# Performance work log

Hardware: AMD Instinct MI355X
Metric: run time of the kernel (lower is better)

The kernel has to match this reference:

```python
import jax, jax.numpy as jnp
import numpy as np

N_NODES = 100000


def gcn_conv(x, edge_index, W, b):
    # PyG GCNConv: add self-loops, symmetric normalization, then scatter-add.
    n = x.shape[0]
    loops = jnp.arange(n, dtype=edge_index.dtype)
    src = jnp.concatenate([edge_index[0], loops])
    dst = jnp.concatenate([edge_index[1], loops])
    h = x @ W  # [N, F_out] -- transform before propagate (small GEMM)
    ones = jnp.ones(src.shape[0], dtype=x.dtype)
    deg = jax.ops.segment_sum(ones, dst, num_segments=n)  # in-degree incl. self-loop
    dinv = jnp.where(deg > 0, jax.lax.rsqrt(deg), 0.0)
    norm = dinv[src] * dinv[dst]  # [E+N]
    msg = h[src] * norm[:, None]  # gather + scale, [E+N, F_out]
    out = jax.ops.segment_sum(msg, dst, num_segments=n)  # scatter-add
    return out + b


def setup_inputs() -> dict:
    key = jax.random.key(0)
    k1, k2, k3, k4 = jax.random.split(key, 4)
    d = 128
    x = jax.random.normal(k1, (N_NODES, d), dtype=jnp.float32)
    edge_index = jax.random.randint(k2, (2, 1600000), 0, N_NODES, dtype=jnp.int64)
    scale = 1.0 / np.sqrt(d)
    W1 = jax.random.normal(k3, (d, d), dtype=jnp.float32) * scale
    b1 = jnp.zeros((d,), dtype=jnp.float32)
    W2 = jax.random.normal(k4, (d, d), dtype=jnp.float32) * scale
    b2 = jnp.zeros((d,), dtype=jnp.float32)
    return {"x": x, "edge_index": edge_index, "W1": W1, "b1": b1, "W2": W2, "b2": b2}


def reference(x, edge_index, W1, b1, W2, b2):
    # Layer 1: GCNConv -> relu -> dropout(eval: identity)
    h = jax.nn.relu(gcn_conv(x, edge_index, W1, b1))
    # Layer 2
    h = jax.nn.relu(gcn_conv(h, edge_index, W2, b2))
    return h
```

## Files before the change

### kernel.cpp

```cpp
#include <hip/hip_runtime.h>


#define NFEAT 128
#define BSH 7
#define MAXNB 1024
#define BCAP 4096
#define BPITCH 136

typedef __attribute__((ext_vector_type(8))) short s8v;
typedef __attribute__((ext_vector_type(4))) float f4v;
typedef __attribute__((ext_vector_type(2))) float f2v;

__device__ inline ushort f2bf(float f) {
    union { float f; uint u; } x; x.f = f;
    uint u = x.u;
    return (ushort)((u + 0x7fffu + ((u >> 16) & 1u)) >> 16);
}
__device__ inline float bf16lo(uint u) { union { uint u; float f; } x; x.u = u << 16; return x.f; }
__device__ inline float bf16hi(uint u) { union { uint u; float f; } x; x.u = u & 0xffff0000u; return x.f; }
__device__ inline f2v unpk(uint u) {
    union { uint u; float f; } lo, hi;
    lo.u = u << 16;
    hi.u = u & 0xffff0000u;
    return (f2v){lo.f, hi.f};
}
__device__ inline void upadd2(uint4 v, f2v* a) {
    a[0] += unpk(v.x);
    a[1] += unpk(v.y);
    a[2] += unpk(v.z);
    a[3] += unpk(v.w);
}

__global__ __launch_bounds__(256) void k_bscatter(const int* __restrict__ src,
                                                  const int* __restrict__ dst,
                                                  int* __restrict__ gcnt,
                                                  uint* __restrict__ ebuf,
                                                  int E, int NB, int CH) {
    __shared__ int h[MAXNB];
    int t = threadIdx.x;
    for (int i = t; i < NB; i += 256) h[i] = 0;
    __syncthreads();
    int e0 = blockIdx.x * CH;
    int e1 = min(e0 + CH, E);
    for (int e = e0 + t; e < e1; e += 256) atomicAdd(&h[dst[e] >> BSH], 1);
    __syncthreads();
    for (int i = t; i < NB; i += 256) {
        int c = h[i];
        h[i] = c ? (i * BCAP + atomicAdd(&gcnt[i], c)) : 0;
    }
    __syncthreads();
    for (int e = e0 + t; e < e1; e += 256) {
        int d = dst[e];
        int b = d >> BSH;
        int p = atomicAdd(&h[b], 1);
        if (p < (b + 1) * BCAP)
            ebuf[p] = ((uint)src[e] << BSH) | (uint)(d & ((1 << BSH) - 1));
    }
}

__global__ __launch_bounds__(256) void k_fill2(const uint* __restrict__ ebuf,
                                               const int* __restrict__ gcnt,
                                               int* __restrict__ row_ptr,
                                               float* __restrict__ dinv,
                                               int* __restrict__ col,
                                               int N, int E, int NB) {
    __shared__ int cnt[128];
    __shared__ int pre[128];
    __shared__ int sred[256];
    __shared__ int colL[BCAP];
    int b = blockIdx.x;
    int t = threadIdx.x;
    int part = 0;
    for (int j = t; j < b; j += 256) part += gcnt[j];
    sred[t] = part;
    __syncthreads();
    for (int off = 128; off >= 1; off >>= 1) {
        if (t < off) sred[t] += sred[t + off];
        __syncthreads();
    }
    int gb = sred[0];
    int m = min(gcnt[b], BCAP);
    if (t < 128) cnt[t] = 0;
    __syncthreads();
    const uint* eb = ebuf + (size_t)b * BCAP;
    for (int i = t; i < m; i += 256) atomicAdd(&cnt[eb[i] & 127], 1);
    __syncthreads();
    if (t < 128) pre[t] = cnt[t];
    __syncthreads();
    for (int off = 1; off < 128; off <<= 1) {
        int add = (t >= off && t < 128) ? pre[t - off] : 0;
        __syncthreads();
        if (t < 128) pre[t] += add;
        __syncthreads();
    }
    if (t < 128) {
        pre[t] -= cnt[t];
        int node = (b << BSH) + t;
        if (node < N) {
            row_ptr[node] = gb + pre[t];
            dinv[node] = rsqrtf((float)(cnt[t] + 1));
        }
    }
    __syncthreads();
    for (int i = t; i < m; i += 256) {
        uint p = eb[i];
        int pos = atomicAdd(&pre[p & 127], 1);
        colL[pos] = (int)(p >> BSH);
    }
    __syncthreads();
    for (int i = t; i < m; i += 256) col[gb + i] = colL[i];
    if (b == NB - 1 && t == 0) row_ptr[N] = E;
}

template <bool ABF16>
__global__ __launch_bounds__(256) void k_gemm3(const void* __restrict__ Ap,
                                               const float* __restrict__ W,
                                               const float* __restrict__ dinv,
                                               ushort* __restrict__ hs, int M) {
    __shared__ ushort Bs[128 * BPITCH];
    int t = threadIdx.x;
    if (blockIdx.x == 0 && t < 64) ((uint*)(hs + (size_t)M * NFEAT))[t] = 0;

#pragma unroll
    for (int i = 0; i < 16; i++) {
        int idx = t + i * 256;
        int k4 = idx >> 7;
        int n = idx & 127;
        ushort o[4];
#pragma unroll
        for (int j = 0; j < 4; j++) o[j] = f2bf(W[(k4 * 4 + j) * NFEAT + n]);
        uint2 pk;
        __builtin_memcpy(&pk, o, 8);
        *(uint2*)&Bs[n * BPITCH + k4 * 4] = pk;
    }
    __syncthreads();

    int w = t >> 6, l = t & 63;
    int q = l >> 4, ln = l & 15;
    int wid = blockIdx.x * 4 + w;
    int row0 = wid * 32;
    bool alive = row0 < M;
    if (!alive) row0 = (M - 32) & ~31;

    s8v afr[2][4];
#pragma unroll
    for (int mt = 0; mt < 2; mt++) {
        int row = row0 + mt * 16 + ln;
        if (row >= M) row = M - 1;
        if (ABF16) {
            const ushort* A = (const ushort*)Ap + (size_t)row * NFEAT + q * 8;
#pragma unroll
            for (int ks = 0; ks < 4; ks++)
                afr[mt][ks] = *(const s8v*)(A + ks * 32);
        } else {
            const float* A = (const float*)Ap + (size_t)row * NFEAT + q * 8;
#pragma unroll
            for (int ks = 0; ks < 4; ks++) {
                float4 f0 = *(const float4*)(A + ks * 32);
                float4 f1 = *(const float4*)(A + ks * 32 + 4);
                ushort o[8] = {f2bf(f0.x), f2bf(f0.y), f2bf(f0.z), f2bf(f0.w),
                               f2bf(f1.x), f2bf(f1.y), f2bf(f1.z), f2bf(f1.w)};
                __builtin_memcpy(&afr[mt][ks], o, 16);
            }
        }
    }

    f4v acc[2][8];
#pragma unroll
    for (int mt = 0; mt < 2; mt++)
#pragma unroll
        for (int nt = 0; nt < 8; nt++) acc[mt][nt] = (f4v){0.f, 0.f, 0.f, 0.f};
#pragma unroll
    for (int nt = 0; nt < 8; nt++) {
        const ushort* Bp = Bs + (nt * 16 + ln) * BPITCH + q * 8;
#pragma unroll
        for (int ks = 0; ks < 4; ks++) {
            s8v bfr = *(const s8v*)(Bp + ks * 32);
            acc[0][nt] = __builtin_amdgcn_mfma_f32_16x16x32_bf16(afr[0][ks], bfr, acc[0][nt], 0, 0, 0);
            acc[1][nt] = __builtin_amdgcn_mfma_f32_16x16x32_bf16(afr[1][ks], bfr, acc[1][nt], 0, 0, 0);
        }
    }
    __syncthreads();

    ushort* ow = Bs + w * 32 * NFEAT;
#pragma unroll
    for (int mt = 0; mt < 2; mt++) {
#pragma unroll
        for (int r = 0; r < 4; r++) {
            int lrow = mt * 16 + q * 4 + r;
            float d = dinv[row0 + lrow];
#pragma unroll
            for (int nt = 0; nt < 8; nt++)
                ow[lrow * NFEAT + nt * 16 + ln] = f2bf(acc[mt][nt][r] * d);
        }
    }
    __builtin_amdgcn_s_waitcnt(0);
#pragma unroll
    for (int i = 0; i < 8; i++) {
        int idx = l + i * 64;
        int r = idx >> 4, c = idx & 15;
        uint4 v = *(uint4*)(ow + r * NFEAT + c * 8);
        if (alive) *(uint4*)(hs + (size_t)(row0 + r) * NFEAT + c * 8) = v;
    }
}

template <bool OUT_BF16>
__global__ __launch_bounds__(256) void k_aggregate(const uint4* __restrict__ hs4,
                                                   const int* __restrict__ row_ptr,
                                                   const int* __restrict__ col,
                                                   const float* __restrict__ dinv,
                                                   const float* __restrict__ bias,
                                                   void* __restrict__ outp, int N) {
    int i = blockIdx.x * 4 + (threadIdx.x >> 6);
    if (i >= N) return;
    int lane = threadIdx.x & 63;
    int g = lane >> 4, sub = lane & 15;
    f2v a[4];
#pragma unroll
    for (int j = 0; j < 4; j++) a[j] = (f2v){0.f, 0.f};
    if (g == 0) upadd2(hs4[(size_t)i * 16 + sub], a);
    int s = row_ptr[i], e = row_ptr[i + 1];
    int k = s;
    for (; k + 16 <= e; k += 16) {
        int c0 = col[k + g];
        int c1 = col[k + 4 + g];
        int c2 = col[k + 8 + g];
        int c3 = col[k + 12 + g];
        uint4 v0 = hs4[(size_t)c0 * 16 + sub];
        uint4 v1 = hs4[(size_t)c1 * 16 + sub];
        uint4 v2 = hs4[(size_t)c2 * 16 + sub];
        uint4 v3 = hs4[(size_t)c3 * 16 + sub];
        upadd2(v0, a); upadd2(v1, a); upadd2(v2, a); upadd2(v3, a);
    }
    for (; k < e; k += 4) {
        int idx = k + g;
        int c = N;
        if (idx < e) c = col[idx];
        upadd2(hs4[(size_t)c * 16 + sub], a);
    }
#pragma unroll
    for (int j = 0; j < 4; j++) {
        a[j].x += __shfl_xor(a[j].x, 16, 64);
        a[j].y += __shfl_xor(a[j].y, 16, 64);
        a[j].x += __shfl_xor(a[j].x, 32, 64);
        a[j].y += __shfl_xor(a[j].y, 32, 64);
    }
    if (lane < 16) {
        float di = dinv[i];
        const float4* b4 = (const float4*)bias;
        float4 b0 = b4[sub * 2], b1 = b4[sub * 2 + 1];
        float r[8];
        r[0] = fmaxf(fmaf(di, a[0].x, b0.x), 0.f);
        r[1] = fmaxf(fmaf(di, a[0].y, b0.y), 0.f);
        r[2] = fmaxf(fmaf(di, a[1].x, b0.z), 0.f);
        r[3] = fmaxf(fmaf(di, a[1].y, b0.w), 0.f);
        r[4] = fmaxf(fmaf(di, a[2].x, b1.x), 0.f);
        r[5] = fmaxf(fmaf(di, a[2].y, b1.y), 0.f);
        r[6] = fmaxf(fmaf(di, a[3].x, b1.z), 0.f);
        r[7] = fmaxf(fmaf(di, a[3].y, b1.w), 0.f);
        if (OUT_BF16) {
            ushort o[8];
#pragma unroll
            for (int j = 0; j < 8; j++) o[j] = f2bf(r[j]);
            uint4 pk;
            __builtin_memcpy(&pk, o, 16);
            ((uint4*)outp)[(size_t)i * 16 + sub] = pk;
        } else {
            float* orow = (float*)outp + (size_t)i * NFEAT + sub * 8;
            *(float4*)orow = make_float4(r[0], r[1], r[2], r[3]);
            *(float4*)(orow + 4) = make_float4(r[4], r[5], r[6], r[7]);
        }
    }
}

extern "C" void kernel_launch(void* const* d_in, const int* in_sizes, int n_in,
                              void* d_out, int out_size, void* d_ws, size_t ws_size,
                              hipStream_t stream) {
    const float* x = (const float*)d_in[0];
    const int* ei = (const int*)d_in[1];
    const float* W1 = (const float*)d_in[2];
    const float* b1 = (const float*)d_in[3];
    const float* W2 = (const float*)d_in[4];
    const float* b2 = (const float*)d_in[5];
    float* out = (float*)d_out;

    const int N = in_sizes[0] / NFEAT;
    const int E = in_sizes[1] / 2;
    const int* src = ei;
    const int* dst = ei + E;
    const int NB = (N + (1 << BSH) - 1) >> BSH;

    char* w = (char*)d_ws;
    size_t off = 0;
    auto alloc = [&](size_t bytes) -> void* {
        void* p = w + off;
        off = (off + bytes + 511) & ~(size_t)511;
        return p;
    };
    ushort* hs = (ushort*)alloc((size_t)(N + 1) * NFEAT * 2);
    ushort* y1 = (ushort*)alloc((size_t)N * NFEAT * 2);
    int* row_ptr = (int*)alloc((size_t)(N + 1) * 4);
    float* dinv = (float*)alloc((size_t)N * 4);
    int* col = (int*)alloc((size_t)E * 4);
    uint* ebuf = (uint*)alloc((size_t)NB * BCAP * 4);
    int* gcnt = (int*)alloc((size_t)MAXNB * 4);
    (void)ws_size; (void)n_in; (void)out_size;

    const int CH = 2048;
    const int chBlk = (E + CH - 1) / CH;

    hipMemsetAsync(gcnt, 0, (size_t)MAXNB * 4, stream);
    k_bscatter<<<chBlk, 256, 0, stream>>>(src, dst, gcnt, ebuf, E, NB, CH);
    k_fill2<<<NB, 256, 0, stream>>>(ebuf, gcnt, row_ptr, dinv, col, N, E, NB);

    const int gemmBlk = (N + 127) / 128;
    const int aggBlk = (N + 3) / 4;

    k_gemm3<false><<<gemmBlk, 256, 0, stream>>>(x, W1, dinv, hs, N);
    k_aggregate<true><<<aggBlk, 256, 0, stream>>>((const uint4*)hs, row_ptr, col, dinv, b1, y1, N);
    k_gemm3<true><<<gemmBlk, 256, 0, stream>>>(y1, W2, dinv, hs, N);
    k_aggregate<false><<<aggBlk, 256, 0, stream>>>((const uint4*)hs, row_ptr, col, dinv, b2, out, N);
}
```

Baseline: 314.6 us.

## Assign one 16-lane group per node in aggregation and pad GEMM epilogue LDS

The aggregate kernel now gives each node a 16-lane group instead of a full 64-lane wavefront, so each block handles 16 nodes. This removes the cross-group shuffle reduction, the idle lanes in the epilogue, and the zero-padding row used for tail edges. The cost is less memory-level parallelism per node, since each node now has only 4 neighbor gathers in flight per unrolled step. Separately, the GEMM epilogue staging in shared memory uses a padded pitch of 132 to reduce bank conflicts, at the price of splitting each 16-byte read into two 8-byte reads.

Result: faster. 303.0 us (-3.7%).

```diff
diff --git a/kernel.cpp b/kernel.cpp
--- a/kernel.cpp
+++ b/kernel.cpp
@@ -6,6 +6,7 @@
 #define MAXNB 1024
 #define BCAP 4096
 #define BPITCH 136
+#define EPITCH 132
 
 typedef __attribute__((ext_vector_type(8))) short s8v;
 typedef __attribute__((ext_vector_type(4))) float f4v;
@@ -16,8 +17,6 @@
     uint u = x.u;
     return (ushort)((u + 0x7fffu + ((u >> 16) & 1u)) >> 16);
 }
-__device__ inline float bf16lo(uint u) { union { uint u; float f; } x; x.u = u << 16; return x.f; }
-__device__ inline float bf16hi(uint u) { union { uint u; float f; } x; x.u = u & 0xffff0000u; return x.f; }
 __device__ inline f2v unpk(uint u) {
     union { uint u; float f; } lo, hi;
     lo.u = u << 16;
@@ -119,7 +118,6 @@
                                                ushort* __restrict__ hs, int M) {
     __shared__ ushort Bs[128 * BPITCH];
     int t = threadIdx.x;
-    if (blockIdx.x == 0 && t < 64) ((uint*)(hs + (size_t)M * NFEAT))[t] = 0;
 
 #pragma unroll
     for (int i = 0; i < 16; i++) {
@@ -182,7 +180,7 @@
     }
     __syncthreads();
 
-    ushort* ow = Bs + w * 32 * NFEAT;
+    ushort* ow = Bs + w * 32 * EPITCH;
 #pragma unroll
     for (int mt = 0; mt < 2; mt++) {
 #pragma unroll
@@ -191,7 +189,7 @@
             float d = dinv[row0 + lrow];
 #pragma unroll
             for (int nt = 0; nt < 8; nt++)
-                ow[lrow * NFEAT + nt * 16 + ln] = f2bf(acc[mt][nt][r] * d);
+                ow[lrow * EPITCH + nt * 16 + ln] = f2bf(acc[mt][nt][r] * d);
         }
     }
     __builtin_amdgcn_s_waitcnt(0);
@@ -199,7 +197,10 @@
     for (int i = 0; i < 8; i++) {
         int idx = l + i * 64;
         int r = idx >> 4, c = idx & 15;
-        uint4 v = *(uint4*)(ow + r * NFEAT + c * 8);
+        const ushort* p = ow + r * EPITCH + c * 8;
+        uint2 lo = *(const uint2*)p;
+        uint2 hi = *(const uint2*)(p + 4);
+        uint4 v = make_uint4(lo.x, lo.y, hi.x, hi.y);
         if (alive) *(uint4*)(hs + (size_t)(row0 + r) * NFEAT + c * 8) = v;
     }
 }
@@ -211,65 +212,48 @@
                                                    const float* __restrict__ dinv,
                                                    const float* __restrict__ bias,
                                                    void* __restrict__ outp, int N) {
-    int i = blockIdx.x * 4 + (threadIdx.x >> 6);
-    if (i >= N) return;
-    int lane = threadIdx.x & 63;
-    int g = lane >> 4, sub = lane & 15;
+    int node = blockIdx.x * 16 + (threadIdx.x >> 4);
+    if (node >= N) return;
+    int sub = threadIdx.x & 15;
     f2v a[4];
 #pragma unroll
     for (int j = 0; j < 4; j++) a[j] = (f2v){0.f, 0.f};
-    if (g == 0) upadd2(hs4[(size_t)i * 16 + sub], a);
-    int s = row_ptr[i], e = row_ptr[i + 1];
+    upadd2(hs4[(size_t)node * 16 + sub], a);
+    int s = row_ptr[node], e = row_ptr[node + 1];
     int k = s;
-    for (; k + 16 <= e; k += 16) {
-        int c0 = col[k + g];
-        int c1 = col[k + 4 + g];
-        int c2 = col[k + 8 + g];
-        int c3 = col[k + 12 + g];
+    for (; k + 4 <= e; k += 4) {
+        int c0 = col[k], c1 = col[k + 1], c2 = col[k + 2], c3 = col[k + 3];
         uint4 v0 = hs4[(size_t)c0 * 16 + sub];
         uint4 v1 = hs4[(size_t)c1 * 16 + sub];
         uint4 v2 = hs4[(size_t)c2 * 16 + sub];
         uint4 v3 = hs4[(size_t)c3 * 16 + sub];
         upadd2(v0, a); upadd2(v1, a); upadd2(v2, a); upadd2(v3, a);
     }
-    for (; k < e; k += 4) {
-        int idx = k + g;
-        int c = N;
-        if (idx < e) c = col[idx];
-        upadd2(hs4[(size_t)c * 16 + sub], a);
-    }
-#pragma unroll
-    for (int j = 0; j < 4; j++) {
-        a[j].x += __shfl_xor(a[j].x, 16, 64);
-        a[j].y += __shfl_xor(a[j].y, 16, 64);
-        a[j].x += __shfl_xor(a[j].x, 32, 64);
-        a[j].y += __shfl_xor(a[j].y, 32, 64);
-    }
-    if (lane < 16) {
-        float di = dinv[i];
-        const float4* b4 = (const float4*)bias;
-        float4 b0 = b4[sub * 2], b1 = b4[sub * 2 + 1];
-        float r[8];
-        r[0] = fmaxf(fmaf(di, a[0].x, b0.x), 0.f);
-        r[1] = fmaxf(fmaf(di, a[0].y, b0.y), 0.f);
-        r[2] = fmaxf(fmaf(di, a[1].x, b0.z), 0.f);
-        r[3] = fmaxf(fmaf(di, a[1].y, b0.w), 0.f);
-        r[4] = fmaxf(fmaf(di, a[2].x, b1.x), 0.f);
-        r[5] = fmaxf(fmaf(di, a[2].y, b1.y), 0.f);
-        r[6] = fmaxf(fmaf(di, a[3].x, b1.z), 0.f);
-        r[7] = fmaxf(fmaf(di, a[3].y, b1.w), 0.f);
-        if (OUT_BF16) {
-            ushort o[8];
-#pragma unroll
-            for (int j = 0; j < 8; j++) o[j] = f2bf(r[j]);
-            uint4 pk;
-            __builtin_memcpy(&pk, o, 16);
-            ((uint4*)outp)[(size_t)i * 16 + sub] = pk;
-        } else {
-            float* orow = (float*)outp + (size_t)i * NFEAT + sub * 8;
-            *(float4*)orow = make_float4(r[0], r[1], r[2], r[3]);
-            *(float4*)(orow + 4) = make_float4(r[4], r[5], r[6], r[7]);
-        }
+    for (; k < e; ++k) upadd2(hs4[(size_t)col[k] * 16 + sub], a);
+
+    float di = dinv[node];
+    const float4* b4 = (const float4*)bias;
+    float4 b0 = b4[sub * 2], b1 = b4[sub * 2 + 1];
+    float r[8];
+    r[0] = fmaxf(fmaf(di, a[0].x, b0.x), 0.f);
+    r[1] = fmaxf(fmaf(di, a[0].y, b0.y), 0.f);
+    r[2] = fmaxf(fmaf(di, a[1].x, b0.z), 0.f);
+    r[3] = fmaxf(fmaf(di, a[1].y, b0.w), 0.f);
+    r[4] = fmaxf(fmaf(di, a[2].x, b1.x), 0.f);
+    r[5] = fmaxf(fmaf(di, a[2].y, b1.y), 0.f);
+    r[6] = fmaxf(fmaf(di, a[3].x, b1.z), 0.f);
+    r[7] = fmaxf(fmaf(di, a[3].y, b1.w), 0.f);
+    if (OUT_BF16) {
+        ushort o[8];
+#pragma unroll
+        for (int j = 0; j < 8; j++) o[j] = f2bf(r[j]);
+        uint4 pk;
+        __builtin_memcpy(&pk, o, 16);
+        ((uint4*)outp)[(size_t)node * 16 + sub] = pk;
+    } else {
+        float* orow = (float*)outp + (size_t)node * NFEAT + sub * 8;
+        *(float4*)orow = make_float4(r[0], r[1], r[2], r[3]);
+        *(float4*)(orow + 4) = make_float4(r[4], r[5], r[6], r[7]);
     }
 }
 
@@ -297,7 +281,7 @@
         off = (off + bytes + 511) & ~(size_t)511;
         return p;
     };
-    ushort* hs = (ushort*)alloc((size_t)(N + 1) * NFEAT * 2);
+    ushort* hs = (ushort*)alloc((size_t)N * NFEAT * 2);
     ushort* y1 = (ushort*)alloc((size_t)N * NFEAT * 2);
     int* row_ptr = (int*)alloc((size_t)(N + 1) * 4);
     float* dinv = (float*)alloc((size_t)N * 4);
@@ -314,7 +298,7 @@
     k_fill2<<<NB, 256, 0, stream>>>(ebuf, gcnt, row_ptr, dinv, col, N, E, NB);
 
     const int gemmBlk = (N + 127) / 128;
-    const int aggBlk = (N + 3) / 4;
+    const int aggBlk = (N + 15) / 16;
 
     k_gemm3<false><<<gemmBlk, 256, 0, stream>>>(x, W1, dinv, hs, N);
     k_aggregate<true><<<aggBlk, 256, 0, stream>>>((const uint4*)hs, row_ptr, col, dinv, b1, y1, N);
```
